# Performance work log

Hardware: AMD Instinct MI355X
Metric: run time of the kernel (lower is better)

Reference implementation:

```python
import jax, jax.numpy as jnp
import numpy as np

D = 256
FF = 1024
NH = 8
BZ, TL = 8, 1024
L, Hs, Ws = 1, 64, 64


def _linear(x, w, b):
    # torch nn.Linear convention: w is [out, in]
    return x @ w.T + b


def _ln(x, g, b, eps=1e-5):
    m = x.mean(-1, keepdims=True)
    v = ((x - m) ** 2).mean(-1, keepdims=True)
    return (x - m) / jnp.sqrt(v + eps) * g + b


def setup_inputs() -> dict:
    key = jax.random.key(0)
    ks = jax.random.split(key, 16)
    s = 0.02
    inp = {
        "tgt": jax.random.normal(ks[0], (BZ, TL, D), jnp.float32),
        "reference_points": jax.random.uniform(ks[1], (BZ, TL, 2), jnp.float32),
        "srcs": jax.random.normal(ks[2], (BZ, L, D, Hs, Ws), jnp.float32),
        "posemb_2d": jax.random.normal(ks[3], (BZ, TL, D), jnp.float32),
        # self-attn (nn.MultiheadAttention) params
        "in_proj_w": jax.random.normal(ks[4], (3 * D, D), jnp.float32) * s,
        "in_proj_b": jnp.zeros((3 * D,), jnp.float32),
        "out_proj_w": jax.random.normal(ks[5], (D, D), jnp.float32) * s,
        "out_proj_b": jnp.zeros((D,), jnp.float32),
        # hand-rolled cross-attn linears (q, k, v, out)
        "lin_q_w": jax.random.normal(ks[6], (D, D), jnp.float32) * s,
        "lin_q_b": jnp.zeros((D,), jnp.float32),
        "lin_k_w": jax.random.normal(ks[7], (D, D), jnp.float32) * s,
        "lin_k_b": jnp.zeros((D,), jnp.float32),
        "lin_v_w": jax.random.normal(ks[8], (D, D), jnp.float32) * s,
        "lin_v_b": jnp.zeros((D,), jnp.float32),
        "lin_o_w": jax.random.normal(ks[9], (D, D), jnp.float32) * s,
        "lin_o_b": jnp.zeros((D,), jnp.float32),
        # layer norms
        "norm1_g": jnp.ones((D,), jnp.float32),
        "norm1_b": jnp.zeros((D,), jnp.float32),
        "norm2_g": jnp.ones((D,), jnp.float32),
        "norm2_b": jnp.zeros((D,), jnp.float32),
        # FFN
        "ffn_w1": jax.random.normal(ks[10], (FF, D), jnp.float32) * s,
        "ffn_b1": jnp.zeros((FF,), jnp.float32),
        "ffn_w2": jax.random.normal(ks[11], (D, FF), jnp.float32) * s,
        "ffn_b2": jnp.zeros((D,), jnp.float32),
        "ffn_norm_g": jnp.ones((D,), jnp.float32),
        "ffn_norm_b": jnp.zeros((D,), jnp.float32),
    }
    return inp


def reference(tgt, reference_points, srcs, posemb_2d,
              in_proj_w, in_proj_b, out_proj_w, out_proj_b,
              lin_q_w, lin_q_b, lin_k_w, lin_k_b, lin_v_w, lin_v_b,
              lin_o_w, lin_o_b,
              norm1_g, norm1_b, norm2_g, norm2_b,
              ffn_w1, ffn_b1, ffn_w2, ffn_b2, ffn_norm_g, ffn_norm_b):
    bz, tl, c = tgt.shape
    nh = NH
    dh = c // nh
    scale = dh ** -0.5

    # ---- self-attention (nn.MultiheadAttention math) ----
    qk = tgt + posemb_2d  # q = k = with_pos_embed(tgt, posemb_2d_)
    wq, wk, wv = in_proj_w[:c], in_proj_w[c:2 * c], in_proj_w[2 * c:]
    bq, bk, bv = in_proj_b[:c], in_proj_b[c:2 * c], in_proj_b[2 * c:]
    qp = _linear(qk, wq, bq).reshape(bz, tl, nh, dh)
    kp = _linear(qk, wk, bk).reshape(bz, tl, nh, dh)
    vp = _linear(tgt, wv, bv).reshape(bz, tl, nh, dh)
    att = jax.nn.softmax(jnp.einsum('bqhd,bkhd->bhqk', qp * scale, kp), axis=-1)
    sa = jnp.einsum('bhqk,bkhd->bqhd', att, vp).reshape(bz, tl, c)
    sa = _linear(sa, out_proj_w, out_proj_b)
    tgt = _ln(tgt + sa, norm2_g, norm2_b)

    # ---- hand-rolled cross attention ----
    bz_, l, c_, h, w = srcs.shape
    s = jnp.transpose(srcs.reshape(bz_ * l, c_, h, w), (0, 2, 3, 1)).reshape(bz_ * l, h * w, c_)
    query = _linear(tgt, lin_q_w, lin_q_b)          # [bz, tl, c]
    key = _linear(s, lin_k_w, lin_k_b)              # [bz*l, hw, c]
    value = _linear(s, lin_v_w, lin_v_b)
    affinity = jax.nn.softmax(jnp.einsum('bqc,bkc->bqk', query, key), axis=-1)  # no 1/sqrt(d) scale, faithful
    tgt2 = _linear(jnp.einsum('bqk,bkc->bqc', affinity, value), lin_o_w, lin_o_b)
    tgt = _ln(tgt + tgt2, norm1_g, norm1_b)

    # ---- FFN ----
    src2 = _linear(jax.nn.relu(_linear(tgt, ffn_w1, ffn_b1)), ffn_w2, ffn_b2)
    tgt = _ln(tgt + src2, ffn_norm_g, ffn_norm_b)
    return tgt
```

## Files before the change

### kernel.cpp

```cpp
#include <hip/hip_runtime.h>
#include <hip/hip_bf16.h>
#include <math.h>

typedef __attribute__((ext_vector_type(8))) __bf16 bf16x8;
typedef __attribute__((ext_vector_type(4))) __bf16 bf16x4;
typedef __attribute__((ext_vector_type(2))) __bf16 bf16x2;
typedef __attribute__((ext_vector_type(4))) float  f32x4;

#define MFMA16(a,b,c) __builtin_amdgcn_mfma_f32_16x16x32_bf16((a),(b),(c),0,0,0)

__device__ __forceinline__ float wave16_max(float v){
  v = fmaxf(v, __shfl_xor(v,1));
  v = fmaxf(v, __shfl_xor(v,2));
  v = fmaxf(v, __shfl_xor(v,4));
  v = fmaxf(v, __shfl_xor(v,8));
  return v;
}
__device__ __forceinline__ float wave16_sum(float v){
  v += __shfl_xor(v,1);
  v += __shfl_xor(v,2);
  v += __shfl_xor(v,4);
  v += __shfl_xor(v,8);
  return v;
}
__device__ __forceinline__ unsigned pack2bf(float a, float b){
  bf16x2 t; t[0] = (__bf16)a; t[1] = (__bf16)b;
  return __builtin_bit_cast(unsigned, t);
}

template<bool RELU, bool BF16OUT>
__global__ __launch_bounds__(256) void gemm_bt(
    const float* __restrict__ A, const float* __restrict__ W,
    const float* __restrict__ bias, void* __restrict__ Cv,
    int M, int N, int K, int ldc, int coff)
{
  __shared__ __align__(16) __bf16 As[128][40];
  __shared__ __align__(16) __bf16 Bs[64][40];

  const int tid  = threadIdx.x;
  const int wid  = tid >> 6;
  const int lane = tid & 63;
  const int wr   = wid >> 1;
  const int wc   = wid & 1;
  const int lq   = lane & 15;
  const int lk8  = (lane >> 4) << 3;
  const int rb   = (lane >> 4) << 2;

  const int m0 = blockIdx.x * 128;
  const int n0 = blockIdx.y * 64;

  const int scg = (tid & 7) << 2;
  const int sr  = tid >> 3;

  f32x4 acc[4][2];
  #pragma unroll
  for (int i=0;i<4;i++)
    #pragma unroll
    for (int j=0;j<2;j++) acc[i][j] = f32x4{0.f,0.f,0.f,0.f};

  for (int k0=0; k0<K; k0+=32){
    __syncthreads();
    #pragma unroll
    for (int i=0;i<4;i++){
      const int row = sr + i*32;
      const float4 a4 = *(const float4*)&A[(size_t)(m0+row)*K + k0 + scg];
      bf16x4 h; h[0]=(__bf16)a4.x; h[1]=(__bf16)a4.y; h[2]=(__bf16)a4.z; h[3]=(__bf16)a4.w;
      *(bf16x4*)&As[row][scg] = h;
    }
    #pragma unroll
    for (int i=0;i<2;i++){
      const int row = sr + i*32;
      const float4 a4 = *(const float4*)&W[(size_t)(n0+row)*K + k0 + scg];
      bf16x4 h; h[0]=(__bf16)a4.x; h[1]=(__bf16)a4.y; h[2]=(__bf16)a4.z; h[3]=(__bf16)a4.w;
      *(bf16x4*)&Bs[row][scg] = h;
    }
    __syncthreads();
    bf16x8 af[4], bfr[2];
    #pragma unroll
    for (int i=0;i<4;i++) af[i]  = *(const bf16x8*)&As[wr*64 + i*16 + lq][lk8];
    #pragma unroll
    for (int j=0;j<2;j++) bfr[j] = *(const bf16x8*)&Bs[wc*32 + j*16 + lq][lk8];
    #pragma unroll
    for (int i=0;i<4;i++)
      #pragma unroll
      for (int j=0;j<2;j++)
        acc[i][j] = MFMA16(af[i], bfr[j], acc[i][j]);
  }

  #pragma unroll
  for (int i=0;i<4;i++)
    #pragma unroll
    for (int j=0;j<2;j++){
      const int coln = n0 + wc*32 + j*16 + lq;
      const float bv = bias ? bias[coln] : 0.f;
      #pragma unroll
      for (int r=0;r<4;r++){
        const int rowm = m0 + wr*64 + i*16 + rb + r;
        float vv = acc[i][j][r] + bv;
        if (RELU) vv = fmaxf(vv, 0.f);
        const size_t idx = (size_t)rowm*ldc + coff + coln;
        if (BF16OUT) ((__bf16*)Cv)[idx] = (__bf16)vv;
        else         ((float*)Cv)[idx]  = vv;
      }
    }
}

template<bool TRANSOUT>
__global__ __launch_bounds__(256) void gemm_srcs(
    const float* __restrict__ S, const float* __restrict__ W,
    const float* __restrict__ bias, __bf16* __restrict__ C)
{
  __shared__ __align__(16) __bf16 As[128][40];
  __shared__ __align__(16) __bf16 Bs[64][40];

  const int tid  = threadIdx.x;
  const int wid  = tid >> 6;
  const int lane = tid & 63;
  const int wr   = wid >> 1;
  const int wc   = wid & 1;
  const int lq   = lane & 15;
  const int lk8  = (lane >> 4) << 3;
  const int rb   = (lane >> 4) << 2;

  const int m0 = blockIdx.x * 128;
  const int n0 = blockIdx.y * 64;
  const int bb = m0 >> 12;
  const int p0 = m0 & 4095;

  const int cA = tid & 31;
  const int qA = tid >> 5;
  const int scg = (tid & 7) << 2;
  const int sr  = tid >> 3;

  f32x4 acc[4][2];
  #pragma unroll
  for (int i=0;i<4;i++)
    #pragma unroll
    for (int j=0;j<2;j++) acc[i][j] = f32x4{0.f,0.f,0.f,0.f};

  for (int k0=0; k0<256; k0+=32){
    __syncthreads();
    const float* sbase = &S[((size_t)bb*256 + k0 + cA)*4096 + p0];
    #pragma unroll
    for (int ps=0; ps<4; ps++){
      const int p = ps*32 + qA*4;
      const float4 f4 = *(const float4*)(sbase + p);
      As[p+0][cA] = (__bf16)f4.x;
      As[p+1][cA] = (__bf16)f4.y;
      As[p+2][cA] = (__bf16)f4.z;
      As[p+3][cA] = (__bf16)f4.w;
    }
    #pragma unroll
    for (int i=0;i<2;i++){
      const int row = sr + i*32;
      const float4 a4 = *(const float4*)&W[(size_t)(n0+row)*256 + k0 + scg];
      bf16x4 h; h[0]=(__bf16)a4.x; h[1]=(__bf16)a4.y; h[2]=(__bf16)a4.z; h[3]=(__bf16)a4.w;
      *(bf16x4*)&Bs[row][scg] = h;
    }
    __syncthreads();
    bf16x8 af[4], bfr[2];
    #pragma unroll
    for (int i=0;i<4;i++) af[i]  = *(const bf16x8*)&As[wr*64 + i*16 + lq][lk8];
    #pragma unroll
    for (int j=0;j<2;j++) bfr[j] = *(const bf16x8*)&Bs[wc*32 + j*16 + lq][lk8];
    #pragma unroll
    for (int i=0;i<4;i++)
      #pragma unroll
      for (int j=0;j<2;j++)
        acc[i][j] = MFMA16(af[i], bfr[j], acc[i][j]);
  }

  #pragma unroll
  for (int i=0;i<4;i++)
    #pragma unroll
    for (int j=0;j<2;j++){
      const int coln = n0 + wc*32 + j*16 + lq;
      const float bv = bias ? bias[coln] : 0.f;
      if (TRANSOUT){
        bf16x4 hv;
        #pragma unroll
        for (int r=0;r<4;r++) hv[r] = (__bf16)(acc[i][j][r] + bv);
        *(bf16x4*)&C[((size_t)bb*256 + coln)*4096 + p0 + wr*64 + i*16 + rb] = hv;
      } else {
        #pragma unroll
        for (int r=0;r<4;r++){
          const int rowm = m0 + wr*64 + i*16 + rb + r;
          C[(size_t)rowm*256 + coln] = (__bf16)(acc[i][j][r] + bv);
        }
      }
    }
}

__global__ __launch_bounds__(256) void add_vec4(const float* __restrict__ a,
                                                const float* __restrict__ b,
                                                float* __restrict__ o, int n4)
{
  const int i = blockIdx.x*blockDim.x + threadIdx.x;
  if (i < n4){
    const float4 x = ((const float4*)a)[i];
    const float4 y = ((const float4*)b)[i];
    float4 z; z.x=x.x+y.x; z.y=x.y+y.y; z.z=x.z+y.z; z.w=x.w+y.w;
    ((float4*)o)[i] = z;
  }
}

__global__ __launch_bounds__(256) void ln_kernel(const float* __restrict__ res,
                                                 const float* __restrict__ x,
                                                 const float* __restrict__ g,
                                                 const float* __restrict__ beta,
                                                 float* __restrict__ out)
{
  const int row  = blockIdx.x*4 + (threadIdx.x >> 6);
  const int lane = threadIdx.x & 63;
  const int c = lane*4;
  const float4 rv = *(const float4*)&res[(size_t)row*256 + c];
  const float4 xv = *(const float4*)&x[(size_t)row*256 + c];
  float v0=rv.x+xv.x, v1=rv.y+xv.y, v2=rv.z+xv.z, v3=rv.w+xv.w;
  float s = v0+v1+v2+v3;
  #pragma unroll
  for (int off=1; off<64; off<<=1) s += __shfl_xor(s, off);
  const float mean = s * (1.f/256.f);
  const float d0=v0-mean, d1=v1-mean, d2=v2-mean, d3=v3-mean;
  float q = d0*d0 + d1*d1 + d2*d2 + d3*d3;
  #pragma unroll
  for (int off=1; off<64; off<<=1) q += __shfl_xor(q, off);
  const float rstd = rsqrtf(q*(1.f/256.f) + 1e-5f);
  const float4 gv = *(const float4*)&g[c];
  const float4 bv = *(const float4*)&beta[c];
  float4 ov;
  ov.x = d0*rstd*gv.x + bv.x;
  ov.y = d1*rstd*gv.y + bv.y;
  ov.z = d2*rstd*gv.z + bv.z;
  ov.w = d3*rstd*gv.w + bv.w;
  *(float4*)&out[(size_t)row*256 + c] = ov;
}

__global__ __launch_bounds__(256) void flash_self(const __bf16* __restrict__ qkv,
                                                  float* __restrict__ sa)
{
  const int qt = blockIdx.x;
  const int b  = blockIdx.y >> 3;
  const int h  = blockIdx.y & 7;
  const int tid  = threadIdx.x;
  const int wid  = tid >> 6;
  const int lane = tid & 63;
  const int lq   = lane & 15;
  const int lk8  = (lane >> 4) << 3;
  const int rb   = (lane >> 4) << 2;

  __shared__ __align__(16) __bf16 Vt[32][40];
  __shared__ __align__(16) __bf16 Pl[4][16][40];

  const int qrow = b*1024 + qt*64 + wid*16 + lq;
  const bf16x8 qf = *(const bf16x8*)&qkv[(size_t)qrow*768 + h*32 + lk8];

  float m[4], l[4];
  f32x4 o[2];
  #pragma unroll
  for (int r=0;r<4;r++){ m[r] = -1e30f; l[r] = 0.f; }
  o[0] = f32x4{0.f,0.f,0.f,0.f};
  o[1] = f32x4{0.f,0.f,0.f,0.f};

  const int vk = tid & 31;
  const int vd = (tid >> 5) << 2;
  const float scale = 0.17677669529663687f;

  for (int kc=0; kc<32; ++kc){
    const int key0 = kc*32;
    __syncthreads();
    {
      const bf16x4 vv = *(const bf16x4*)&qkv[(size_t)(b*1024 + key0 + vk)*768 + 512 + h*32 + vd];
      #pragma unroll
      for (int j=0;j<4;j++) Vt[vd+j][vk] = vv[j];
    }
    const __bf16* kbase = &qkv[(size_t)(b*1024 + key0)*768 + 256 + h*32 + lk8];
    const bf16x8 kf0 = *(const bf16x8*)(kbase + (size_t)lq*768);
    const bf16x8 kf1 = *(const bf16x8*)(kbase + (size_t)(16+lq)*768);
    const f32x4 z = f32x4{0.f,0.f,0.f,0.f};
    const f32x4 s0 = MFMA16(qf, kf0, z);
    const f32x4 s1 = MFMA16(qf, kf1, z);
    #pragma unroll
    for (int r=0;r<4;r++){
      const float a0 = s0[r]*scale, a1 = s1[r]*scale;
      const float mx = wave16_max(fmaxf(a0,a1));
      const float mn = fmaxf(m[r], mx);
      const float alpha = __expf(m[r]-mn);
      const float p0 = __expf(a0-mn);
      const float p1 = __expf(a1-mn);
      const float rs = wave16_sum(p0+p1);
      l[r] = l[r]*alpha + rs;
      o[0][r] *= alpha;
      o[1][r] *= alpha;
      m[r] = mn;
      Pl[wid][rb+r][lq]      = (__bf16)p0;
      Pl[wid][rb+r][16+lq]   = (__bf16)p1;
    }
    __syncthreads();
    const bf16x8 pf  = *(const bf16x8*)&Pl[wid][lq][lk8];
    const bf16x8 vf0 = *(const bf16x8*)&Vt[lq][lk8];
    const bf16x8 vf1 = *(const bf16x8*)&Vt[16+lq][lk8];
    o[0] = MFMA16(pf, vf0, o[0]);
    o[1] = MFMA16(pf, vf1, o[1]);
  }
  #pragma unroll
  for (int nf=0;nf<2;nf++)
    #pragma unroll
    for (int r=0;r<4;r++){
      const int row = b*1024 + qt*64 + wid*16 + rb + r;
      sa[(size_t)row*256 + h*32 + nf*16 + lq] = o[nf][r] / l[r];
    }
}

__global__ __launch_bounds__(256, 2) void flash_cross(
    const __bf16* __restrict__ qg, const __bf16* __restrict__ kg,
    const __bf16* __restrict__ vtg, float* __restrict__ Opart,
    float* __restrict__ ml)
{
  extern __shared__ __bf16 smem[];
  __bf16* Ks = smem;
  __bf16* Vt = smem + 64*256;

  const int qt = blockIdx.x;
  const int b  = blockIdx.y;
  const int sl = blockIdx.z;
  const int tid  = threadIdx.x;
  const int wid  = tid >> 6;
  const int lane = tid & 63;
  const int lq   = lane & 15;
  const int hi   = lane >> 4;
  const int lk8  = hi << 3;
  const int rb   = hi << 2;
  const int swz  = lq & 7;

  const int qrow = b*1024 + qt*64 + wid*16 + lq;
  bf16x8 qf[8];
  #pragma unroll
  for (int ks=0; ks<8; ks++)
    qf[ks] = *(const bf16x8*)&qg[(size_t)qrow*256 + ks*32 + lk8];

  float m = -1e30f, l = 0.f;
  f32x4 o[16];
  #pragma unroll
  for (int nf=0; nf<16; nf++) o[nf] = f32x4{0.f,0.f,0.f,0.f};

  const int srow = tid >> 2;
  const int sc4  = tid & 3;

  for (int it=0; it<16; ++it){
    const int key0 = sl*1024 + it*64;
    __syncthreads();
    {
      const __bf16* kb = &kg[(size_t)(b*4096 + key0 + srow)*256];
      #pragma unroll
      for (int j=0;j<8;j++){
        const int ch = sc4 + j*4;
        const bf16x8 vv = *(const bf16x8*)(kb + ch*8);
        *(bf16x8*)&Ks[srow*256 + ((ch ^ (srow&7))<<3)] = vv;
      }
    }
    {
      #pragma unroll
      for (int ps=0; ps<4; ps++){
        const int d = srow + ps*64;
        const __bf16* vb = &vtg[(size_t)(b*256 + d)*4096 + key0];
        #pragma unroll
        for (int s2=0;s2<2;s2++){
          const int ch = sc4 + s2*4;
          const bf16x8 vv = *(const bf16x8*)(vb + ch*8);
          *(bf16x8*)&Vt[d*64 + ((ch ^ (d&7))<<3)] = vv;
        }
      }
    }
    __syncthreads();
    f32x4 s4[4];
    #pragma unroll
    for (int kt=0;kt<4;kt++) s4[kt] = f32x4{0.f,0.f,0.f,0.f};
    #pragma unroll
    for (int ks=0; ks<8; ks++){
      #pragma unroll
      for (int kt=0; kt<4; kt++){
        const bf16x8 kf = *(const bf16x8*)&Ks[(kt*16+lq)*256 + (((ks*4+hi) ^ swz)<<3)];
        s4[kt] = MFMA16(kf, qf[ks], s4[kt]);
      }
    }
    float pm = s4[0][0];
    #pragma unroll
    for (int kt=0;kt<4;kt++)
      #pragma unroll
      for (int r=0;r<4;r++) pm = fmaxf(pm, s4[kt][r]);
    pm = fmaxf(pm, __shfl_xor(pm, 16));
    pm = fmaxf(pm, __shfl_xor(pm, 32));
    if (!__all(pm <= m + 8.f)){
      const float mn = fmaxf(m, pm);
      const float alpha = __expf(m - mn);
      #pragma unroll
      for (int nf=0;nf<16;nf++){
        o[nf][0]*=alpha; o[nf][1]*=alpha; o[nf][2]*=alpha; o[nf][3]*=alpha;
      }
      l *= alpha;
      m = mn;
    }
    float p[4][4];
    float rs = 0.f;
    #pragma unroll
    for (int kt=0;kt<4;kt++)
      #pragma unroll
      for (int r=0;r<4;r++){ p[kt][r] = __expf(s4[kt][r] - m); rs += p[kt][r]; }
    rs += __shfl_xor(rs, 16);
    rs += __shfl_xor(rs, 32);
    l += rs;
    unsigned pk0[4], pk1[4];
    #pragma unroll
    for (int kt=0;kt<4;kt++){
      pk0[kt] = pack2bf(p[kt][0], p[kt][1]);
      pk1[kt] = pack2bf(p[kt][2], p[kt][3]);
    }
    const int srcA = ((hi&1)<<5) + lq;
    const int srcB = srcA + 16;
    const bool ksel = hi >= 2;
    bf16x8 pf[2];
    #pragma unroll
    for (int ks2=0; ks2<2; ks2++){
      const unsigned a0 = (unsigned)__shfl((int)pk0[2*ks2],   srcA);
      const unsigned a1 = (unsigned)__shfl((int)pk0[2*ks2+1], srcA);
      const unsigned b0 = (unsigned)__shfl((int)pk1[2*ks2],   srcA);
      const unsigned b1 = (unsigned)__shfl((int)pk1[2*ks2+1], srcA);
      const unsigned c0 = (unsigned)__shfl((int)pk0[2*ks2],   srcB);
      const unsigned c1 = (unsigned)__shfl((int)pk0[2*ks2+1], srcB);
      const unsigned d0 = (unsigned)__shfl((int)pk1[2*ks2],   srcB);
      const unsigned d1 = (unsigned)__shfl((int)pk1[2*ks2+1], srcB);
      union { unsigned u[4]; bf16x8 v; } uu;
      uu.u[0] = ksel ? a1 : a0;
      uu.u[1] = ksel ? b1 : b0;
      uu.u[2] = ksel ? c1 : c0;
      uu.u[3] = ksel ? d1 : d0;
      pf[ks2] = uu.v;
    }
    #pragma unroll
    for (int nf=0; nf<16; nf++){
      #pragma unroll
      for (int ks2=0; ks2<2; ks2++){
        const bf16x8 af = *(const bf16x8*)&Vt[(nf*16+lq)*64 + (((ks2*4+hi) ^ swz)<<3)];
        o[nf] = MFMA16(af, pf[ks2], o[nf]);
      }
    }
  }
  const int row = b*1024 + qt*64 + wid*16 + lq;
  if (hi == 0){
    ml[(size_t)(sl*8192 + row)*2 + 0] = m;
    ml[(size_t)(sl*8192 + row)*2 + 1] = l;
  }
  #pragma unroll
  for (int nf=0; nf<16; nf++)
    *(f32x4*)&Opart[(size_t)(sl*8192 + row)*256 + nf*16 + rb] = o[nf];
}

__global__ __launch_bounds__(256) void combine_kernel(const float* __restrict__ Opart,
                                                      const float* __restrict__ ml,
                                                      float* __restrict__ out)
{
  const int row = blockIdx.x;
  const int d = threadIdx.x;
  float mm[4], ll[4];
  #pragma unroll
  for (int s=0;s<4;s++){
    mm[s] = ml[(size_t)(s*8192+row)*2 + 0];
    ll[s] = ml[(size_t)(s*8192+row)*2 + 1];
  }
  const float M = fmaxf(fmaxf(mm[0],mm[1]), fmaxf(mm[2],mm[3]));
  float L = 0.f, acc = 0.f;
  #pragma unroll
  for (int s=0;s<4;s++){
    const float e = __expf(mm[s]-M);
    L   += ll[s]*e;
    acc += e * Opart[(size_t)(s*8192+row)*256 + d];
  }
  out[(size_t)row*256 + d] = acc / L;
}

extern "C" void kernel_launch(void* const* d_in, const int* in_sizes, int n_in,
                              void* d_out, int out_size, void* d_ws, size_t ws_size,
                              hipStream_t stream)
{
  (void)in_sizes; (void)n_in; (void)out_size; (void)ws_size;
  const float* tgt        = (const float*)d_in[0];
  const float* srcs       = (const float*)d_in[2];
  const float* posemb     = (const float*)d_in[3];
  const float* in_proj_w  = (const float*)d_in[4];
  const float* in_proj_b  = (const float*)d_in[5];
  const float* out_proj_w = (const float*)d_in[6];
  const float* out_proj_b = (const float*)d_in[7];
  const float* lin_q_w    = (const float*)d_in[8];
  const float* lin_q_b    = (const float*)d_in[9];
  const float* lin_k_w    = (const float*)d_in[10];
  const float* lin_k_b    = (const float*)d_in[11];
  const float* lin_v_w    = (const float*)d_in[12];
  const float* lin_v_b    = (const float*)d_in[13];
  const float* lin_o_w    = (const float*)d_in[14];
  const float* lin_o_b    = (const float*)d_in[15];
  const float* norm1_g    = (const float*)d_in[16];
  const float* norm1_b    = (const float*)d_in[17];
  const float* norm2_g    = (const float*)d_in[18];
  const float* norm2_b    = (const float*)d_in[19];
  const float* ffn_w1     = (const float*)d_in[20];
  const float* ffn_b1     = (const float*)d_in[21];
  const float* ffn_w2     = (const float*)d_in[22];
  const float* ffn_b2     = (const float*)d_in[23];
  const float* ffn_norm_g = (const float*)d_in[24];
  const float* ffn_norm_b = (const float*)d_in[25];
  float* out = (float*)d_out;

  char* w = (char*)d_ws;
  const size_t MB = (size_t)1 << 20;
  float*  tgt1    = (float*)(w + 0);
  float*  qk      = (float*)(w + 8*MB);
  float*  sa      = (float*)(w + 8*MB);
  __bf16* query_b = (__bf16*)(w + 8*MB);
  float*  attn2   = (float*)(w + 8*MB);
  __bf16* qkv     = (__bf16*)(w + 16*MB);
  float*  saproj  = (float*)(w + 16*MB);
  __bf16* key_b   = (__bf16*)(w + 16*MB);
  float*  t2proj  = (float*)(w + 16*MB);
  float*  tgt3    = (float*)(w + 24*MB);
  __bf16* val_t   = (__bf16*)(w + 32*MB);
  float*  ffn_h   = (float*)(w + 32*MB);
  float*  Opart   = (float*)(w + 48*MB);
  float*  ffn_out = (float*)(w + 64*MB);
  float*  ml      = (float*)(w + 82*MB);

  add_vec4<<<2048,256,0,stream>>>(tgt, posemb, qk, (8*1024*256)/4);
  gemm_bt<false,true><<<dim3(64,8),256,0,stream>>>(qk, in_proj_w, in_proj_b,
      qkv, 8192,512,256, 768,0);
  gemm_bt<false,true><<<dim3(64,4),256,0,stream>>>(tgt, in_proj_w + 512*256,
      in_proj_b + 512, qkv, 8192,256,256, 768,512);
  flash_self<<<dim3(16,64),256,0,stream>>>(qkv, sa);
  gemm_bt<false,false><<<dim3(64,4),256,0,stream>>>(sa, out_proj_w, out_proj_b,
      saproj, 8192,256,256, 256,0);
  ln_kernel<<<2048,256,0,stream>>>(tgt, saproj, norm2_g, norm2_b, tgt1);

  gemm_bt<false,true><<<dim3(64,4),256,0,stream>>>(tgt1, lin_q_w, lin_q_b,
      query_b, 8192,256,256, 256,0);
  gemm_srcs<false><<<dim3(256,4),256,0,stream>>>(srcs, lin_k_w, lin_k_b, key_b);
  gemm_srcs<true ><<<dim3(256,4),256,0,stream>>>(srcs, lin_v_w, lin_v_b, val_t);
  flash_cross<<<dim3(16,8,4),256,65536,stream>>>(query_b, key_b, val_t, Opart, ml);
  combine_kernel<<<8192,256,0,stream>>>(Opart, ml, attn2);
  gemm_bt<false,false><<<dim3(64,4),256,0,stream>>>(attn2, lin_o_w, lin_o_b,
      t2proj, 8192,256,256, 256,0);
  ln_kernel<<<2048,256,0,stream>>>(tgt1, t2proj, norm1_g, norm1_b, tgt3);

  gemm_bt<true,false><<<dim3(64,16),256,0,stream>>>(tgt3, ffn_w1, ffn_b1,
      ffn_h, 8192,1024,256, 1024,0);
  gemm_bt<false,false><<<dim3(64,4),256,0,stream>>>(ffn_h, ffn_w2, ffn_b2,
      ffn_out, 8192,256,1024, 256,0);
  ln_kernel<<<2048,256,0,stream>>>(tgt3, ffn_out, ffn_norm_g, ffn_norm_b, out);
}
```

Before: 322.8 us.

## Restructure self-attention with separate Q/K/V-transposed buffers and register-resident softmax

Self-attention Q, K and V are now produced into separate bf16 buffers. Q is pre-scaled in the GEMM epilogue and V is written transposed. This lets flash_self load K and V fragments straight from global memory without shared-memory staging or barriers. The kernel processes 64 keys per iteration, skips the online-softmax rescale unless the max grows by more than 8, and moves P between lanes with shuffles instead of LDS. Separately, most 256-wide GEMMs switch to 64-row tiles to launch twice as many blocks, at the cost of less operand reuse per block.

Result: faster. 297.1 us (-8.0%).

```diff
diff --git a/kernel.cpp b/kernel.cpp
--- a/kernel.cpp
+++ b/kernel.cpp
@@ -9,32 +9,19 @@
 
 #define MFMA16(a,b,c) __builtin_amdgcn_mfma_f32_16x16x32_bf16((a),(b),(c),0,0,0)
 
-__device__ __forceinline__ float wave16_max(float v){
-  v = fmaxf(v, __shfl_xor(v,1));
-  v = fmaxf(v, __shfl_xor(v,2));
-  v = fmaxf(v, __shfl_xor(v,4));
-  v = fmaxf(v, __shfl_xor(v,8));
-  return v;
-}
-__device__ __forceinline__ float wave16_sum(float v){
-  v += __shfl_xor(v,1);
-  v += __shfl_xor(v,2);
-  v += __shfl_xor(v,4);
-  v += __shfl_xor(v,8);
-  return v;
-}
 __device__ __forceinline__ unsigned pack2bf(float a, float b){
   bf16x2 t; t[0] = (__bf16)a; t[1] = (__bf16)b;
   return __builtin_bit_cast(unsigned, t);
 }
 
-template<bool RELU, bool BF16OUT>
+template<int BM, bool RELU, int OUTMODE>
 __global__ __launch_bounds__(256) void gemm_bt(
     const float* __restrict__ A, const float* __restrict__ W,
     const float* __restrict__ bias, void* __restrict__ Cv,
-    int M, int N, int K, int ldc, int coff)
-{
-  __shared__ __align__(16) __bf16 As[128][40];
+    int M, int N, int K, int ldc, int coff, float oscale)
+{
+  constexpr int MT = BM/32;
+  __shared__ __align__(16) __bf16 As[BM][40];
   __shared__ __align__(16) __bf16 Bs[64][40];
 
   const int tid  = threadIdx.x;
@@ -46,22 +33,22 @@
   const int lk8  = (lane >> 4) << 3;
   const int rb   = (lane >> 4) << 2;
 
-  const int m0 = blockIdx.x * 128;
+  const int m0 = blockIdx.x * BM;
   const int n0 = blockIdx.y * 64;
 
   const int scg = (tid & 7) << 2;
   const int sr  = tid >> 3;
 
-  f32x4 acc[4][2];
-  #pragma unroll
-  for (int i=0;i<4;i++)
+  f32x4 acc[MT][2];
+  #pragma unroll
+  for (int i=0;i<MT;i++)
     #pragma unroll
     for (int j=0;j<2;j++) acc[i][j] = f32x4{0.f,0.f,0.f,0.f};
 
   for (int k0=0; k0<K; k0+=32){
     __syncthreads();
     #pragma unroll
-    for (int i=0;i<4;i++){
+    for (int i=0;i<MT;i++){
       const int row = sr + i*32;
       const float4 a4 = *(const float4*)&A[(size_t)(m0+row)*K + k0 + scg];
       bf16x4 h; h[0]=(__bf16)a4.x; h[1]=(__bf16)a4.y; h[2]=(__bf16)a4.z; h[3]=(__bf16)a4.w;
@@ -75,32 +62,44 @@
       *(bf16x4*)&Bs[row][scg] = h;
     }
     __syncthreads();
-    bf16x8 af[4], bfr[2];
-    #pragma unroll
-    for (int i=0;i<4;i++) af[i]  = *(const bf16x8*)&As[wr*64 + i*16 + lq][lk8];
-    #pragma unroll
-    for (int j=0;j<2;j++) bfr[j] = *(const bf16x8*)&Bs[wc*32 + j*16 + lq][lk8];
-    #pragma unroll
-    for (int i=0;i<4;i++)
+    bf16x8 af[MT], bfr[2];
+    #pragma unroll
+    for (int i=0;i<MT;i++) af[i]  = *(const bf16x8*)&As[wr*(BM/2) + i*16 + lq][lk8];
+    #pragma unroll
+    for (int j=0;j<2;j++)  bfr[j] = *(const bf16x8*)&Bs[wc*32 + j*16 + lq][lk8];
+    #pragma unroll
+    for (int i=0;i<MT;i++)
       #pragma unroll
       for (int j=0;j<2;j++)
         acc[i][j] = MFMA16(af[i], bfr[j], acc[i][j]);
   }
 
   #pragma unroll
-  for (int i=0;i<4;i++)
+  for (int i=0;i<MT;i++)
     #pragma unroll
     for (int j=0;j<2;j++){
       const int coln = n0 + wc*32 + j*16 + lq;
       const float bv = bias ? bias[coln] : 0.f;
-      #pragma unroll
-      for (int r=0;r<4;r++){
-        const int rowm = m0 + wr*64 + i*16 + rb + r;
-        float vv = acc[i][j][r] + bv;
-        if (RELU) vv = fmaxf(vv, 0.f);
-        const size_t idx = (size_t)rowm*ldc + coff + coln;
-        if (BF16OUT) ((__bf16*)Cv)[idx] = (__bf16)vv;
-        else         ((float*)Cv)[idx]  = vv;
+      if (OUTMODE == 2){
+        const int rowm0 = m0 + wr*(BM/2) + i*16 + rb;
+        bf16x4 hv;
+        #pragma unroll
+        for (int r=0;r<4;r++){
+          float vv = (acc[i][j][r] + bv) * oscale;
+          if (RELU) vv = fmaxf(vv, 0.f);
+          hv[r] = (__bf16)vv;
+        }
+        *(bf16x4*)&((__bf16*)Cv)[((size_t)((rowm0>>10)*256) + coln)*1024 + (rowm0&1023)] = hv;
+      } else {
+        #pragma unroll
+        for (int r=0;r<4;r++){
+          const int rowm = m0 + wr*(BM/2) + i*16 + rb + r;
+          float vv = (acc[i][j][r] + bv) * oscale;
+          if (RELU) vv = fmaxf(vv, 0.f);
+          const size_t idx = (size_t)rowm*ldc + coff + coln;
+          if (OUTMODE == 1) ((__bf16*)Cv)[idx] = (__bf16)vv;
+          else              ((float*)Cv)[idx]  = vv;
+        }
       }
     }
 }
@@ -235,8 +234,9 @@
   *(float4*)&out[(size_t)row*256 + c] = ov;
 }
 
-__global__ __launch_bounds__(256) void flash_self(const __bf16* __restrict__ qkv,
-                                                  float* __restrict__ sa)
+__global__ __launch_bounds__(256) void flash_self(
+    const __bf16* __restrict__ qs, const __bf16* __restrict__ ks,
+    const __bf16* __restrict__ vts, float* __restrict__ sa)
 {
   const int qt = blockIdx.x;
   const int b  = blockIdx.y >> 3;
@@ -245,70 +245,92 @@
   const int wid  = tid >> 6;
   const int lane = tid & 63;
   const int lq   = lane & 15;
-  const int lk8  = (lane >> 4) << 3;
-  const int rb   = (lane >> 4) << 2;
-
-  __shared__ __align__(16) __bf16 Vt[32][40];
-  __shared__ __align__(16) __bf16 Pl[4][16][40];
+  const int hi   = lane >> 4;
+  const int lk8  = hi << 3;
+  const int rb   = hi << 2;
 
   const int qrow = b*1024 + qt*64 + wid*16 + lq;
-  const bf16x8 qf = *(const bf16x8*)&qkv[(size_t)qrow*768 + h*32 + lk8];
-
-  float m[4], l[4];
-  f32x4 o[2];
-  #pragma unroll
-  for (int r=0;r<4;r++){ m[r] = -1e30f; l[r] = 0.f; }
-  o[0] = f32x4{0.f,0.f,0.f,0.f};
-  o[1] = f32x4{0.f,0.f,0.f,0.f};
-
-  const int vk = tid & 31;
-  const int vd = (tid >> 5) << 2;
-  const float scale = 0.17677669529663687f;
-
-  for (int kc=0; kc<32; ++kc){
-    const int key0 = kc*32;
-    __syncthreads();
-    {
-      const bf16x4 vv = *(const bf16x4*)&qkv[(size_t)(b*1024 + key0 + vk)*768 + 512 + h*32 + vd];
-      #pragma unroll
-      for (int j=0;j<4;j++) Vt[vd+j][vk] = vv[j];
-    }
-    const __bf16* kbase = &qkv[(size_t)(b*1024 + key0)*768 + 256 + h*32 + lk8];
-    const bf16x8 kf0 = *(const bf16x8*)(kbase + (size_t)lq*768);
-    const bf16x8 kf1 = *(const bf16x8*)(kbase + (size_t)(16+lq)*768);
-    const f32x4 z = f32x4{0.f,0.f,0.f,0.f};
-    const f32x4 s0 = MFMA16(qf, kf0, z);
-    const f32x4 s1 = MFMA16(qf, kf1, z);
-    #pragma unroll
-    for (int r=0;r<4;r++){
-      const float a0 = s0[r]*scale, a1 = s1[r]*scale;
-      const float mx = wave16_max(fmaxf(a0,a1));
-      const float mn = fmaxf(m[r], mx);
-      const float alpha = __expf(m[r]-mn);
-      const float p0 = __expf(a0-mn);
-      const float p1 = __expf(a1-mn);
-      const float rs = wave16_sum(p0+p1);
-      l[r] = l[r]*alpha + rs;
-      o[0][r] *= alpha;
-      o[1][r] *= alpha;
-      m[r] = mn;
-      Pl[wid][rb+r][lq]      = (__bf16)p0;
-      Pl[wid][rb+r][16+lq]   = (__bf16)p1;
-    }
-    __syncthreads();
-    const bf16x8 pf  = *(const bf16x8*)&Pl[wid][lq][lk8];
-    const bf16x8 vf0 = *(const bf16x8*)&Vt[lq][lk8];
-    const bf16x8 vf1 = *(const bf16x8*)&Vt[16+lq][lk8];
-    o[0] = MFMA16(pf, vf0, o[0]);
-    o[1] = MFMA16(pf, vf1, o[1]);
-  }
-  #pragma unroll
-  for (int nf=0;nf<2;nf++)
-    #pragma unroll
-    for (int r=0;r<4;r++){
-      const int row = b*1024 + qt*64 + wid*16 + rb + r;
-      sa[(size_t)row*256 + h*32 + nf*16 + lq] = o[nf][r] / l[r];
-    }
+  const bf16x8 qf = *(const bf16x8*)&qs[(size_t)qrow*256 + h*32 + lk8];
+
+  const __bf16* kb0 = &ks[(size_t)(b*1024 + lq)*256 + h*32 + lk8];
+  const __bf16* vb0 = &vts[(size_t)(b*256 + h*32 + lq)*1024 + lk8];
+
+  const f32x4 Z = {0.f, 0.f, 0.f, 0.f};
+  float m = -1e30f, l = 0.f;
+  f32x4 o0 = Z, o1 = Z;
+
+  for (int it=0; it<16; ++it){
+    const int key0 = it*64;
+    f32x4 s4[4];
+    #pragma unroll
+    for (int kt=0;kt<4;kt++){
+      const bf16x8 kf = *(const bf16x8*)(kb0 + (size_t)(key0 + kt*16)*256);
+      s4[kt] = MFMA16(kf, qf, Z);
+    }
+    float pm = s4[0][0];
+    #pragma unroll
+    for (int kt=0;kt<4;kt++)
+      #pragma unroll
+      for (int r=0;r<4;r++) pm = fmaxf(pm, s4[kt][r]);
+    pm = fmaxf(pm, __shfl_xor(pm,16));
+    pm = fmaxf(pm, __shfl_xor(pm,32));
+    if (!__all(pm <= m + 8.f)){
+      const float mn = fmaxf(m, pm);
+      const float alpha = __expf(m - mn);
+      o0[0]*=alpha; o0[1]*=alpha; o0[2]*=alpha; o0[3]*=alpha;
+      o1[0]*=alpha; o1[1]*=alpha; o1[2]*=alpha; o1[3]*=alpha;
+      l *= alpha;
+      m = mn;
+    }
+    float p[4][4]; float rs = 0.f;
+    #pragma unroll
+    for (int kt=0;kt<4;kt++)
+      #pragma unroll
+      for (int r=0;r<4;r++){ p[kt][r] = __expf(s4[kt][r]-m); rs += p[kt][r]; }
+    rs += __shfl_xor(rs,16);
+    rs += __shfl_xor(rs,32);
+    l += rs;
+    unsigned pk0[4], pk1[4];
+    #pragma unroll
+    for (int kt=0;kt<4;kt++){
+      pk0[kt] = pack2bf(p[kt][0], p[kt][1]);
+      pk1[kt] = pack2bf(p[kt][2], p[kt][3]);
+    }
+    const int srcA = ((hi&1)<<5) + lq;
+    const int srcB = srcA + 16;
+    const bool ksel = hi >= 2;
+    bf16x8 pf[2];
+    #pragma unroll
+    for (int ks2=0; ks2<2; ks2++){
+      const unsigned a0 = (unsigned)__shfl((int)pk0[2*ks2],   srcA);
+      const unsigned a1 = (unsigned)__shfl((int)pk0[2*ks2+1], srcA);
+      const unsigned b0 = (unsigned)__shfl((int)pk1[2*ks2],   srcA);
+      const unsigned b1 = (unsigned)__shfl((int)pk1[2*ks2+1], srcA);
+      const unsigned c0 = (unsigned)__shfl((int)pk0[2*ks2],   srcB);
+      const unsigned c1 = (unsigned)__shfl((int)pk0[2*ks2+1], srcB);
+      const unsigned d0 = (unsigned)__shfl((int)pk1[2*ks2],   srcB);
+      const unsigned d1 = (unsigned)__shfl((int)pk1[2*ks2+1], srcB);
+      union { unsigned u[4]; bf16x8 v; } uu;
+      uu.u[0] = ksel ? a1 : a0;
+      uu.u[1] = ksel ? b1 : b0;
+      uu.u[2] = ksel ? c1 : c0;
+      uu.u[3] = ksel ? d1 : d0;
+      pf[ks2] = uu.v;
+    }
+    #pragma unroll
+    for (int ks2=0; ks2<2; ks2++){
+      const bf16x8 vf0 = *(const bf16x8*)(vb0 + key0 + ks2*32);
+      const bf16x8 vf1 = *(const bf16x8*)(vb0 + (size_t)16*1024 + key0 + ks2*32);
+      o0 = MFMA16(vf0, pf[ks2], o0);
+      o1 = MFMA16(vf1, pf[ks2], o1);
+    }
+  }
+  const float inv = 1.f / l;
+  f32x4 w0, w1;
+  #pragma unroll
+  for (int r=0;r<4;r++){ w0[r] = o0[r]*inv; w1[r] = o1[r]*inv; }
+  *(f32x4*)&sa[(size_t)qrow*256 + h*32 + rb]      = w0;
+  *(f32x4*)&sa[(size_t)qrow*256 + h*32 + 16 + rb] = w1;
 }
 
 __global__ __launch_bounds__(256, 2) void flash_cross(
@@ -338,10 +360,11 @@
   for (int ks=0; ks<8; ks++)
     qf[ks] = *(const bf16x8*)&qg[(size_t)qrow*256 + ks*32 + lk8];
 
+  const f32x4 Z = {0.f, 0.f, 0.f, 0.f};
   float m = -1e30f, l = 0.f;
   f32x4 o[16];
   #pragma unroll
-  for (int nf=0; nf<16; nf++) o[nf] = f32x4{0.f,0.f,0.f,0.f};
+  for (int nf=0; nf<16; nf++) o[nf] = Z;
 
   const int srow = tid >> 2;
   const int sc4  = tid & 3;
@@ -374,7 +397,7 @@
     __syncthreads();
     f32x4 s4[4];
     #pragma unroll
-    for (int kt=0;kt<4;kt++) s4[kt] = f32x4{0.f,0.f,0.f,0.f};
+    for (int kt=0;kt<4;kt++) s4[kt] = Z;
     #pragma unroll
     for (int ks=0; ks<8; ks++){
       #pragma unroll
@@ -517,40 +540,46 @@
   float*  sa      = (float*)(w + 8*MB);
   __bf16* query_b = (__bf16*)(w + 8*MB);
   float*  attn2   = (float*)(w + 8*MB);
-  __bf16* qkv     = (__bf16*)(w + 16*MB);
-  float*  saproj  = (float*)(w + 16*MB);
+  float*  ffn_out = (float*)(w + 8*MB);
+  __bf16* q_s     = (__bf16*)(w + 16*MB);
   __bf16* key_b   = (__bf16*)(w + 16*MB);
   float*  t2proj  = (float*)(w + 16*MB);
+  __bf16* k_s     = (__bf16*)(w + 20*MB);
+  __bf16* v_t     = (__bf16*)(w + 24*MB);
   float*  tgt3    = (float*)(w + 24*MB);
+  float*  saproj  = (float*)(w + 28*MB);
   __bf16* val_t   = (__bf16*)(w + 32*MB);
   float*  ffn_h   = (float*)(w + 32*MB);
   float*  Opart   = (float*)(w + 48*MB);
-  float*  ffn_out = (float*)(w + 64*MB);
   float*  ml      = (float*)(w + 82*MB);
 
+  const float SCALE = 0.17677669529663687f;
+
   add_vec4<<<2048,256,0,stream>>>(tgt, posemb, qk, (8*1024*256)/4);
-  gemm_bt<false,true><<<dim3(64,8),256,0,stream>>>(qk, in_proj_w, in_proj_b,
-      qkv, 8192,512,256, 768,0);
-  gemm_bt<false,true><<<dim3(64,4),256,0,stream>>>(tgt, in_proj_w + 512*256,
-      in_proj_b + 512, qkv, 8192,256,256, 768,512);
-  flash_self<<<dim3(16,64),256,0,stream>>>(qkv, sa);
-  gemm_bt<false,false><<<dim3(64,4),256,0,stream>>>(sa, out_proj_w, out_proj_b,
-      saproj, 8192,256,256, 256,0);
+  gemm_bt<64,false,1><<<dim3(128,4),256,0,stream>>>(qk, in_proj_w, in_proj_b,
+      q_s, 8192,256,256, 256,0, SCALE);
+  gemm_bt<64,false,1><<<dim3(128,4),256,0,stream>>>(qk, in_proj_w + 256*256,
+      in_proj_b + 256, k_s, 8192,256,256, 256,0, 1.f);
+  gemm_bt<64,false,2><<<dim3(128,4),256,0,stream>>>(tgt, in_proj_w + 512*256,
+      in_proj_b + 512, v_t, 8192,256,256, 256,0, 1.f);
+  flash_self<<<dim3(16,64),256,0,stream>>>(q_s, k_s, v_t, sa);
+  gemm_bt<64,false,0><<<dim3(128,4),256,0,stream>>>(sa, out_proj_w, out_proj_b,
+      saproj, 8192,256,256, 256,0, 1.f);
   ln_kernel<<<2048,256,0,stream>>>(tgt, saproj, norm2_g, norm2_b, tgt1);
 
-  gemm_bt<false,true><<<dim3(64,4),256,0,stream>>>(tgt1, lin_q_w, lin_q_b,
-      query_b, 8192,256,256, 256,0);
+  gemm_bt<64,false,1><<<dim3(128,4),256,0,stream>>>(tgt1, lin_q_w, lin_q_b,
+      query_b, 8192,256,256, 256,0, 1.f);
   gemm_srcs<false><<<dim3(256,4),256,0,stream>>>(srcs, lin_k_w, lin_k_b, key_b);
   gemm_srcs<true ><<<dim3(256,4),256,0,stream>>>(srcs, lin_v_w, lin_v_b, val_t);
   flash_cross<<<dim3(16,8,4),256,65536,stream>>>(query_b, key_b, val_t, Opart, ml);
   combine_kernel<<<8192,256,0,stream>>>(Opart, ml, attn2);
-  gemm_bt<false,false><<<dim3(64,4),256,0,stream>>>(attn2, lin_o_w, lin_o_b,
-      t2proj, 8192,256,256, 256,0);
+  gemm_bt<64,false,0><<<dim3(128,4),256,0,stream>>>(attn2, lin_o_w, lin_o_b,
+      t2proj, 8192,256,256, 256,0, 1.f);
   ln_kernel<<<2048,256,0,stream>>>(tgt1, t2proj, norm1_g, norm1_b, tgt3);
 
-  gemm_bt<true,false><<<dim3(64,16),256,0,stream>>>(tgt3, ffn_w1, ffn_b1,
-      ffn_h, 8192,1024,256, 1024,0);
-  gemm_bt<false,false><<<dim3(64,4),256,0,stream>>>(ffn_h, ffn_w2, ffn_b2,
-      ffn_out, 8192,256,1024, 256,0);
+  gemm_bt<128,true,0><<<dim3(64,16),256,0,stream>>>(tgt3, ffn_w1, ffn_b1,
+      ffn_h, 8192,1024,256, 1024,0, 1.f);
+  gemm_bt<64,false,0><<<dim3(128,4),256,0,stream>>>(ffn_h, ffn_w2, ffn_b2,
+      ffn_out, 8192,256,1024, 256,0, 1.f);
   ln_kernel<<<2048,256,0,stream>>>(tgt3, ffn_out, ffn_norm_g, ffn_norm_b, out);
 }
```
